# Kernel optimization log

Hardware: AMD Instinct MI355X
Metric: run time of the kernel (lower is better)

## Reference

```python
import jax, jax.numpy as jnp
import numpy as np

N = 100000
NEG_SLOPE = 0.2
EPS = 1e-16


def _gat_layer(x, W, a_src, a_dst, b, src, dst, heads, dim, concat):
    # Linear projection -> [N, H, D]
    h = (x @ W).reshape(x.shape[0], heads, dim)
    # Per-node attention logits [N, H]
    al_src = jnp.sum(h * a_src[None], axis=-1)
    al_dst = jnp.sum(h * a_dst[None], axis=-1)
    # Per-edge logits, leaky relu (negative_slope=0.2)
    e = al_src[src] + al_dst[dst]                      # [E, H]
    e = jnp.where(e >= 0, e, NEG_SLOPE * e)
    # Scatter softmax over destination neighborhoods
    emax = jax.ops.segment_max(e, dst, num_segments=N)  # [N, H]
    ee = jnp.exp(e - emax[dst])
    denom = jax.ops.segment_sum(ee, dst, num_segments=N)
    alpha = ee / (denom[dst] + EPS)                    # [E, H]
    # Weighted scatter-add aggregation
    msg = h[src] * alpha[:, :, None]                   # [E, H, D]
    out = jax.ops.segment_sum(msg, dst, num_segments=N)  # [N, H, D]
    if concat:
        out = out.reshape(N, heads * dim)
    else:
        out = out.mean(axis=1)
    return out + b


def setup_inputs() -> dict:
    key = jax.random.key(0)
    ks = jax.random.split(key, 10)
    F_in, hid, H, C = 500, 8, 8, 3
    E = 3200000
    x = jax.random.normal(ks[0], (N, F_in), dtype=jnp.float32)
    edge_index = jax.random.randint(ks[1], (2, E), 0, N, dtype=jnp.int64)
    s1 = (1.0 / np.sqrt(F_in)).astype(np.float32)
    s2 = (1.0 / np.sqrt(hid * H)).astype(np.float32)
    return {
        "x": x,
        "edge_index": edge_index,
        "W1": jax.random.normal(ks[2], (F_in, H * hid), dtype=jnp.float32) * s1,
        "att_src1": jax.random.normal(ks[3], (H, hid), dtype=jnp.float32),
        "att_dst1": jax.random.normal(ks[4], (H, hid), dtype=jnp.float32),
        "b1": jnp.zeros((H * hid,), dtype=jnp.float32),
        "W2": jax.random.normal(ks[5], (H * hid, C), dtype=jnp.float32) * s2,
        "att_src2": jax.random.normal(ks[6], (1, C), dtype=jnp.float32),
        "att_dst2": jax.random.normal(ks[7], (1, C), dtype=jnp.float32),
        "b2": jnp.zeros((C,), dtype=jnp.float32),
    }


def reference(x, edge_index, W1, att_src1, att_dst1, b1, W2, att_src2, att_dst2, b2):
    # Add self-loops (PyG GATConv default)
    loop = jnp.arange(N, dtype=edge_index.dtype)
    src = jnp.concatenate([edge_index[0], loop])
    dst = jnp.concatenate([edge_index[1], loop])
    # Layer 1: 8 heads, concat -> [N, 64], ELU
    h = _gat_layer(x, W1, att_src1, att_dst1, b1, src, dst, heads=8, dim=8, concat=True)
    h = jax.nn.elu(h)
    # Layer 2: 1 head, no concat -> [N, 3]
    out = _gat_layer(h, W2, att_src2, att_dst2, b2, src, dst, heads=1, dim=3, concat=False)
    return out, jax.nn.log_softmax(out, axis=1)
```

## Files before the change

### kernel.cpp

```cpp
#include <hip/hip_runtime.h>
#include <hip/hip_bf16.h>


#define F_IN 500
#define HEADS 8
#define HID 8
#define HD 64
#define CLS 3
#define NEG 0.2f
#define EPSV 1e-16f
#define LOG2E 1.44269504088896340736f

#define NBLK_H 256
#define NBKT_MAX 3136

typedef __attribute__((ext_vector_type(8))) short short8v;
typedef __attribute__((ext_vector_type(4))) float f32x4;

__device__ inline short bfs(float v) {
    __hip_bfloat16 b = __float2bfloat16(v);
    return *(short*)&b;
}

__device__ inline int ld_edge(const void* ei, long idx, int is64) {
    return is64 ? (int)((const long long*)ei)[idx] : ((const int*)ei)[idx];
}

__global__ void k_prepW(const float* __restrict__ W1, ushort* __restrict__ W1b2,
                        const int* __restrict__ ei, int* __restrict__ flag) {
    if (blockIdx.x == 0 && threadIdx.x == 0) {
        int z = 0;
        for (int i = 1; i < 16; i += 2) z += (ei[i] == 0) ? 1 : 0;
        *flag = (z == 8) ? 1 : 0;
    }
    int i = blockIdx.x * 256 + threadIdx.x;
    if (i >= 16 * 64 * 32) return;
    int ks = i >> 11;
    int c = (i >> 5) & 63;
    int st = i & 31;
    int q = (st >> 3) ^ ((c >> 1) & 3);
    int k = ks * 32 + q * 8 + (st & 7);
    float v = (k < F_IN) ? W1[k * HD + c] : 0.f;
    __hip_bfloat16 b = __float2bfloat16(v);
    W1b2[i] = *(ushort*)&b;
}

__device__ __forceinline__ void g1_stage(const float* __restrict__ x,
        const ushort* __restrict__ W1b2, char* smem, int buf, int ks,
        int rowb, int N, int lane, int w) {
    const int k0 = ks * 32;
    {
        const ushort* srcB = W1b2 + ks * 2048 + (w * 64 + lane) * 8;
        char* dstB = smem + 16384 + buf * 4096 + w * 1024;
        __builtin_amdgcn_global_load_lds(
            (const __attribute__((address_space(1))) void*)srcB,
            (__attribute__((address_space(3))) void*)dstB, 16, 0, 0);
    }
#pragma unroll
    for (int i = 0; i < 2; ++i) {
        int vt = i * 256 + w * 64 + lane;
        int row = vt >> 3;
        int c = (vt & 7) ^ (row & 7);
        int ke = k0 + c * 4; if (ke > 496) ke = 496;
        int rowg = rowb + row; if (rowg >= N) rowg = N - 1;
        const float* srcA = x + (long)rowg * F_IN + ke;
        char* dstA = smem + buf * 8192 + i * 4096 + w * 1024;
        __builtin_amdgcn_global_load_lds(
            (const __attribute__((address_space(1))) void*)srcA,
            (__attribute__((address_space(3))) void*)dstA, 16, 0, 0);
    }
}

__global__ __launch_bounds__(256) void k_fatA(const float* __restrict__ x,
        const ushort* __restrict__ W1b2,
        const float* __restrict__ asrc, const float* __restrict__ adst,
        float* __restrict__ als, float* __restrict__ ald,
        ushort* __restrict__ h1b, int N,
        const void* ei, int E, int nbkt, int* __restrict__ ghist,
        const int* __restrict__ flag) {
    __shared__ char smem[24576];
    int gB = (N + 63) >> 6;
    int t = threadIdx.x;

    if ((int)blockIdx.x >= gB) {
        int hb = blockIdx.x - gB;
        int* h = (int*)smem;
        int tot = E + N;
        int epb = (tot + NBLK_H - 1) / NBLK_H;
        int e0 = hb * epb, e1 = min(tot, e0 + epb);
        for (int i = t; i < nbkt; i += 256) h[i] = 0;
        __syncthreads();
        int is64 = *flag;
        for (int e = e0 + t; e < e1; e += 256) {
            int dst = (e < E) ? ld_edge(ei, (long)E + e, is64) : (e - E);
            atomicAdd(&h[dst >> 5], 1);
        }
        __syncthreads();
        for (int i = t; i < nbkt; i += 256)
            ghist[hb * nbkt + i] = h[i];
        return;
    }

    int lane = t & 63;
    int w = t >> 6;
    int l16 = lane & 15, oct = lane >> 4;
    int rowb = blockIdx.x * 64;

    f32x4 acc0 = {0.f, 0.f, 0.f, 0.f};
    f32x4 acc1 = {0.f, 0.f, 0.f, 0.f};
    f32x4 acc2 = {0.f, 0.f, 0.f, 0.f};
    f32x4 acc3 = {0.f, 0.f, 0.f, 0.f};

    g1_stage(x, W1b2, smem, 0, 0, rowb, N, lane, w);
    __syncthreads();

    int rl = w * 16 + l16;
    int asw = l16 & 7;
    int bsw = (l16 >> 1) & 3;

    for (int ks = 0; ks < 16; ++ks) {
        int cur = ks & 1;
        if (ks < 15)
            g1_stage(x, W1b2, smem, cur ^ 1, ks + 1, rowb, N, lane, w);
        const char* Ab = smem + cur * 8192;
        const char* Bb = smem + 16384 + cur * 4096;
        float4 x0 = *reinterpret_cast<const float4*>(
            Ab + rl * 128 + ((2 * oct + 0) ^ asw) * 16);
        float4 x1 = *reinterpret_cast<const float4*>(
            Ab + rl * 128 + ((2 * oct + 1) ^ asw) * 16);
        short8v a;
        a[0] = bfs(x0.x); a[1] = bfs(x0.y); a[2] = bfs(x0.z); a[3] = bfs(x0.w);
        a[4] = bfs(x1.x); a[5] = bfs(x1.y); a[6] = bfs(x1.z); a[7] = bfs(x1.w);
        short8v b0 = *reinterpret_cast<const short8v*>(
            Bb + (0 * 16 + l16) * 64 + (oct ^ bsw) * 16);
        short8v b1 = *reinterpret_cast<const short8v*>(
            Bb + (1 * 16 + l16) * 64 + (oct ^ bsw) * 16);
        short8v b2 = *reinterpret_cast<const short8v*>(
            Bb + (2 * 16 + l16) * 64 + (oct ^ bsw) * 16);
        short8v b3 = *reinterpret_cast<const short8v*>(
            Bb + (3 * 16 + l16) * 64 + (oct ^ bsw) * 16);
        acc0 = __builtin_amdgcn_mfma_f32_16x16x32_bf16(a, b0, acc0, 0, 0, 0);
        acc1 = __builtin_amdgcn_mfma_f32_16x16x32_bf16(a, b1, acc1, 0, 0, 0);
        acc2 = __builtin_amdgcn_mfma_f32_16x16x32_bf16(a, b2, acc2, 0, 0, 0);
        acc3 = __builtin_amdgcn_mfma_f32_16x16x32_bf16(a, b3, acc3, 0, 0, 0);
        __syncthreads();
    }

    float* fs = (float*)smem;
#pragma unroll
    for (int r = 0; r < 4; ++r) {
        int rl_ = w * 16 + oct * 4 + r;
        fs[rl_ * 64 + l16 +  0] = acc0[r];
        fs[rl_ * 64 + l16 + 16] = acc1[r];
        fs[rl_ * 64 + l16 + 32] = acc2[r];
        fs[rl_ * 64 + l16 + 48] = acc3[r];
    }
    __syncthreads();
#pragma unroll
    for (int j = t; j < 512; j += 256) {
        int row = j >> 3, h = j & 7;
        int gn = rowb + row;
        if (gn < N) {
            const float* hp = fs + row * 64 + h * 8;
            float4 v0 = *reinterpret_cast<const float4*>(hp);
            float4 v1 = *reinterpret_cast<const float4*>(hp + 4);
            const float* s = asrc + h * 8;
            const float* d = adst + h * 8;
            float s1 = v0.x * s[0] + v0.y * s[1] + v0.z * s[2] + v0.w * s[3]
                     + v1.x * s[4] + v1.y * s[5] + v1.z * s[6] + v1.w * s[7];
            float s2 = v0.x * d[0] + v0.y * d[1] + v0.z * d[2] + v0.w * d[3]
                     + v1.x * d[4] + v1.y * d[5] + v1.z * d[6] + v1.w * d[7];
            als[gn * 8 + h] = s1 * LOG2E;
            ald[gn * 8 + h] = s2 * LOG2E;
            ushort hb[8];
            hb[0] = (ushort)bfs(v0.x); hb[1] = (ushort)bfs(v0.y);
            hb[2] = (ushort)bfs(v0.z); hb[3] = (ushort)bfs(v0.w);
            hb[4] = (ushort)bfs(v1.x); hb[5] = (ushort)bfs(v1.y);
            hb[6] = (ushort)bfs(v1.z); hb[7] = (ushort)bfs(v1.w);
            *reinterpret_cast<uint4*>(h1b + (long)gn * HD + h * 8) =
                *reinterpret_cast<const uint4*>(hb);
        }
    }
}


__global__ void k_bsum(int* __restrict__ ghist, int* __restrict__ colsum, int nbkt) {
    int b = blockIdx.x * 256 + threadIdx.x;
    if (b >= nbkt) return;
    int run = 0;
    for (int i = 0; i < NBLK_H; i++) {
        int v = ghist[i * nbkt + b];
        ghist[i * nbkt + b] = run;
        run += v;
    }
    colsum[b] = run;
}

__global__ __launch_bounds__(256) void k_bscan2(const int* __restrict__ colsum,
        int* __restrict__ boff, int nbkt) {
    __shared__ int part[256];
    int per = (nbkt + 255) / 256;
    int t = threadIdx.x;
    int lo = t * per, hi = min(nbkt, lo + per);
    int s = 0;
    for (int i = lo; i < hi; i++) s += colsum[i];
    part[t] = s;
    __syncthreads();
    for (int off = 1; off < 256; off <<= 1) {
        int v = (t >= off) ? part[t - off] : 0;
        __syncthreads();
        part[t] += v;
        __syncthreads();
    }
    int run = (t > 0) ? part[t - 1] : 0;
    for (int i = lo; i < hi; i++) { boff[i] = run; run += colsum[i]; }
    if (t == 255) boff[nbkt] = part[255];
}

__global__ __launch_bounds__(256) void k_scatter(const void* ei, int E, int N, int nbkt,
        const int* __restrict__ ghist, const int* __restrict__ boff,
        uint* __restrict__ pairs, const int* flag) {
    __shared__ int cur[NBKT_MAX];
    int tot = E + N;
    int epb = (tot + NBLK_H - 1) / NBLK_H;
    int e0 = blockIdx.x * epb, e1 = min(tot, e0 + epb);
    for (int i = threadIdx.x; i < nbkt; i += 256)
        cur[i] = boff[i] + ghist[blockIdx.x * nbkt + i];
    __syncthreads();
    int is64 = *flag;
    for (int e = e0 + threadIdx.x; e < e1; e += 256) {
        int src, dst;
        if (e < E) { src = ld_edge(ei, e, is64); dst = ld_edge(ei, (long)E + e, is64); }
        else { src = dst = e - E; }
        int pos = atomicAdd(&cur[dst >> 5], 1);
        pairs[pos] = ((uint)src << 5) | (uint)(dst & 31);
    }
}

__global__ __launch_bounds__(256) void k_fill3(const uint* __restrict__ pairs,
        const int* __restrict__ boff, int* __restrict__ rowptr,
        int* __restrict__ csr, int N, int nbkt) {
    __shared__ int cnt[32];
    __shared__ int base[32];
    __shared__ int cur[32];
    int b = blockIdx.x;
    int t = threadIdx.x;
    if (t < 32) { cnt[t] = 0; cur[t] = 0; }
    __syncthreads();
    int p0 = boff[b], p1 = boff[b + 1];
    for (int p = p0 + t; p < p1; p += 256)
        atomicAdd(&cnt[pairs[p] & 31], 1);
    __syncthreads();
    if (t < 32) {
        int pre = 0;
#pragma unroll
        for (int i = 0; i < 32; i++) pre += (i < t) ? cnt[i] : 0;
        base[t] = p0 + pre;
        int n = b * 32 + t;
        if (n < N) rowptr[n] = base[t];
    }
    if (b == 0 && t == 0) rowptr[N] = boff[nbkt];
    __syncthreads();
    for (int p = p0 + t; p < p1; p += 256) {
        uint v = pairs[p];
        int lo = v & 31;
        int pos = base[lo] + atomicAdd(&cur[lo], 1);
        csr[pos] = (int)(v >> 5);
    }
}

__global__ __launch_bounds__(256) void k_agg1(const int* __restrict__ rowptr,
        const int* __restrict__ csr, const ushort* __restrict__ h1b,
        const float* __restrict__ als, const float* __restrict__ ald,
        const float* __restrict__ b1, const float* __restrict__ W2,
        const float* __restrict__ as2, const float* __restrict__ ad2,
        float* __restrict__ h2p, float* __restrict__ ald2, int N) {
    int lane = threadIdx.x & 63;
    int wid = threadIdx.x >> 6;
    int half = lane >> 5;
    int n = blockIdx.x * 8 + wid * 2 + half;
    bool act = (n < N);
    int nc = act ? n : (N - 1);
    int es = (lane >> 3) & 3;
    int h = lane & 7;
    float aldh = ald[nc * HEADS + h];
    int rs = rowptr[nc], re = rowptr[nc + 1];

    float acc[4][8];
    float den[4] = {0.f, 0.f, 0.f, 0.f};
#pragma unroll
    for (int q = 0; q < 4; ++q)
#pragma unroll
        for (int j = 0; j < 8; ++j) acc[q][j] = 0.f;

    int jb = rs;
    for (; jb + 16 <= re; jb += 16) {
        int s[4]; float e[4]; float p[4]; uint4 u[4];
#pragma unroll
        for (int q = 0; q < 4; ++q) s[q] = csr[jb + q * 4 + es];
#pragma unroll
        for (int q = 0; q < 4; ++q) {
            e[q] = als[s[q] * HEADS + h] + aldh;
            u[q] = *reinterpret_cast<const uint4*>(h1b + (long)s[q] * HD + h * 8);
        }
#pragma unroll
        for (int q = 0; q < 4; ++q) {
            e[q] = fmaxf(e[q], NEG * e[q]);
            p[q] = exp2f(e[q]);
        }
#pragma unroll
        for (int q = 0; q < 4; ++q) {
            acc[q][0] += p[q] * __uint_as_float(u[q].x << 16);
            acc[q][1] += p[q] * __uint_as_float(u[q].x & 0xffff0000u);
            acc[q][2] += p[q] * __uint_as_float(u[q].y << 16);
            acc[q][3] += p[q] * __uint_as_float(u[q].y & 0xffff0000u);
            acc[q][4] += p[q] * __uint_as_float(u[q].z << 16);
            acc[q][5] += p[q] * __uint_as_float(u[q].z & 0xffff0000u);
            acc[q][6] += p[q] * __uint_as_float(u[q].w << 16);
            acc[q][7] += p[q] * __uint_as_float(u[q].w & 0xffff0000u);
            den[q] += p[q];
        }
    }
    for (; jb < re; jb += 4) {
        int eidx = jb + es;
        bool valid = (eidx < re);
        int s = csr[valid ? eidx : rs];
        float e = als[s * HEADS + h] + aldh;
        e = fmaxf(e, NEG * e);
        float p = valid ? exp2f(e) : 0.f;
        uint4 u = *reinterpret_cast<const uint4*>(h1b + (long)s * HD + h * 8);
        acc[0][0] += p * __uint_as_float(u.x << 16);
        acc[0][1] += p * __uint_as_float(u.x & 0xffff0000u);
        acc[0][2] += p * __uint_as_float(u.y << 16);
        acc[0][3] += p * __uint_as_float(u.y & 0xffff0000u);
        acc[0][4] += p * __uint_as_float(u.z << 16);
        acc[0][5] += p * __uint_as_float(u.z & 0xffff0000u);
        acc[0][6] += p * __uint_as_float(u.w << 16);
        acc[0][7] += p * __uint_as_float(u.w & 0xffff0000u);
        den[0] += p;
    }
    float a0 = (acc[0][0] + acc[1][0]) + (acc[2][0] + acc[3][0]);
    float a1 = (acc[0][1] + acc[1][1]) + (acc[2][1] + acc[3][1]);
    float a2 = (acc[0][2] + acc[1][2]) + (acc[2][2] + acc[3][2]);
    float a3 = (acc[0][3] + acc[1][3]) + (acc[2][3] + acc[3][3]);
    float a4 = (acc[0][4] + acc[1][4]) + (acc[2][4] + acc[3][4]);
    float a5 = (acc[0][5] + acc[1][5]) + (acc[2][5] + acc[3][5]);
    float a6 = (acc[0][6] + acc[1][6]) + (acc[2][6] + acc[3][6]);
    float a7 = (acc[0][7] + acc[1][7]) + (acc[2][7] + acc[3][7]);
    float dn = (den[0] + den[1]) + (den[2] + den[3]);
#pragma unroll
    for (int off = 8; off <= 16; off <<= 1) {
        dn += __shfl_xor(dn, off);
        a0 += __shfl_xor(a0, off); a1 += __shfl_xor(a1, off);
        a2 += __shfl_xor(a2, off); a3 += __shfl_xor(a3, off);
        a4 += __shfl_xor(a4, off); a5 += __shfl_xor(a5, off);
        a6 += __shfl_xor(a6, off); a7 += __shfl_xor(a7, off);
    }
    float sel_a = (es < 2) ? ((es == 0) ? a0 : a1) : ((es == 2) ? a2 : a3);
    float sel_b = (es < 2) ? ((es == 0) ? a4 : a5) : ((es == 2) ? a6 : a7);
    int da = h * 8 + es, db = da + 4;
    float inv = 1.f / (dn + EPSV);
    float oa = sel_a * inv + b1[da];
    float ob = sel_b * inv + b1[db];
    oa = (oa > 0.f) ? oa : __expf(oa) - 1.f;
    ob = (ob > 0.f) ? ob : __expf(ob) - 1.f;
    float p0 = oa * W2[da * CLS + 0] + ob * W2[db * CLS + 0];
    float p1 = oa * W2[da * CLS + 1] + ob * W2[db * CLS + 1];
    float p2 = oa * W2[da * CLS + 2] + ob * W2[db * CLS + 2];
#pragma unroll
    for (int off = 1; off <= 16; off <<= 1) {
        p0 += __shfl_xor(p0, off);
        p1 += __shfl_xor(p1, off);
        p2 += __shfl_xor(p2, off);
    }
    if ((lane & 31) == 0 && act) {
        float als2v = (p0 * as2[0] + p1 * as2[1] + p2 * as2[2]) * LOG2E;
        *reinterpret_cast<float4*>(h2p + (long)n * 4) =
            make_float4(p0, p1, p2, als2v);
        ald2[n] = (p0 * ad2[0] + p1 * ad2[1] + p2 * ad2[2]) * LOG2E;
    }
}

__global__ __launch_bounds__(256) void k_agg2(const int* __restrict__ rowptr,
        const int* __restrict__ csr, const float* __restrict__ h2p,
        const float* __restrict__ ald2v,
        const float* __restrict__ b2, float* __restrict__ out, int N) {
    int n = blockIdx.x * 8 + (threadIdx.x >> 5);
    if (n >= N) return;
    int lane = threadIdx.x & 31;
    float aldv = ald2v[n];
    int rs = rowptr[n], re = rowptr[n + 1];
    float sum = 0.f, a0 = 0.f, a1 = 0.f, a2 = 0.f;
    for (int j = rs + lane; j < re; j += 32) {
        int s = csr[j];
        float4 hv = *reinterpret_cast<const float4*>(h2p + (long)s * 4);
        float e = hv.w + aldv;
        e = fmaxf(e, NEG * e);
        float p = exp2f(e);
        sum += p;
        a0 += p * hv.x;
        a1 += p * hv.y;
        a2 += p * hv.z;
    }
#pragma unroll
    for (int off = 1; off < 32; off <<= 1) {
        sum += __shfl_xor(sum, off);
        a0 += __shfl_xor(a0, off);
        a1 += __shfl_xor(a1, off);
        a2 += __shfl_xor(a2, off);
    }
    if (lane == 0) {
        float d = sum + EPSV;
        float v0 = a0 / d + b2[0], v1 = a1 / d + b2[1], v2 = a2 / d + b2[2];
        float mx = fmaxf(v0, fmaxf(v1, v2));
        float se = __expf(v0 - mx) + __expf(v1 - mx) + __expf(v2 - mx);
        float ls = mx + __logf(se);
        out[n * CLS + 0] = v0; out[n * CLS + 1] = v1; out[n * CLS + 2] = v2;
        long o2 = (long)N * CLS;
        out[o2 + n * CLS + 0] = v0 - ls;
        out[o2 + n * CLS + 1] = v1 - ls;
        out[o2 + n * CLS + 2] = v2 - ls;
    }
}

extern "C" void kernel_launch(void* const* d_in, const int* in_sizes, int n_in,
                              void* d_out, int out_size, void* d_ws, size_t ws_size,
                              hipStream_t stream) {
    const float* x   = (const float*)d_in[0];
    const void*  ei  = d_in[1];
    const float* W1  = (const float*)d_in[2];
    const float* as1 = (const float*)d_in[3];
    const float* ad1 = (const float*)d_in[4];
    const float* b1  = (const float*)d_in[5];
    const float* W2  = (const float*)d_in[6];
    const float* as2 = (const float*)d_in[7];
    const float* ad2 = (const float*)d_in[8];
    const float* b2  = (const float*)d_in[9];
    int N = in_sizes[0] / F_IN;
    int E = in_sizes[1] / 2;
    int tot = E + N;
    int nbkt = (N + 31) >> 5;

    char* w = (char*)d_ws;
    auto alloc = [&](size_t bytes) -> char* {
        char* p = w; w += (bytes + 255) & ~size_t(255); return p;
    };
    ushort* h1b    = (ushort*)alloc((size_t)N * HD * 2);
    float*  als1   = (float*)alloc((size_t)N * HEADS * 4);
    float*  ald1   = (float*)alloc((size_t)N * HEADS * 4);
    int*    rowptr = (int*)alloc((size_t)(N + 1) * 4);
    int*    csr    = (int*)alloc((size_t)tot * 4);
    float*  h2p    = (float*)alloc((size_t)N * 4 * 4);
    float*  ald2   = (float*)alloc((size_t)N * 4);
    ushort* W1b2   = (ushort*)alloc((size_t)16 * 64 * 32 * 2);
    int*    flag   = (int*)alloc(256);
    uint*   pairs  = (uint*)alloc((size_t)tot * 4);
    int*    ghist  = (int*)alloc((size_t)NBLK_H * nbkt * 4);
    int*    colsum = (int*)alloc((size_t)nbkt * 4);
    int*    boff   = (int*)alloc((size_t)(nbkt + 1) * 4);

    int gB = (N + 63) / 64;
    k_prepW<<<(16 * 64 * 32 + 255) / 256, 256, 0, stream>>>(W1, W1b2, (const int*)ei, flag);
    k_fatA<<<gB + NBLK_H, 256, 0, stream>>>(x, W1b2, as1, ad1, als1, ald1, h1b, N,
                                            ei, E, nbkt, ghist, flag);
    k_bsum<<<(nbkt + 255) / 256, 256, 0, stream>>>(ghist, colsum, nbkt);
    k_bscan2<<<1, 256, 0, stream>>>(colsum, boff, nbkt);
    k_scatter<<<NBLK_H, 256, 0, stream>>>(ei, E, N, nbkt, ghist, boff, pairs, flag);
    k_fill3<<<nbkt, 256, 0, stream>>>(pairs, boff, rowptr, csr, N, nbkt);
    k_agg1<<<(N + 7) / 8, 256, 0, stream>>>(rowptr, csr, h1b, als1, ald1, b1,
                                            W2, as2, ad2, h2p, ald2, N);
    k_agg2<<<(N + 7) / 8, 256, 0, stream>>>(rowptr, csr, h2p, ald2, b2,
                                            (float*)d_out, N);
}
```

Measured before the change: 298.3 us.

## Fuse CSR bucket fill with layer-1 aggregation in one kernel

Merges the per-bucket CSR fill kernel with the first-layer attention aggregation, so each block finishes building the adjacency for its 32 destination nodes and then aggregates them in four passes. Row bounds come from shared memory instead of a global rowptr reload, and the csr entries just written are likely still in cache. It also drops one kernel launch. In exchange, parallelism falls from about 12.5k blocks to about 3.1k larger blocks, and each block runs its fill and aggregate phases back to back, which may reduce latency hiding for the gather-heavy aggregation.

After: 305.0 us. 1.02x slower.

```diff
diff --git a/kernel.cpp b/kernel.cpp
--- a/kernel.cpp
+++ b/kernel.cpp
@@ -237,11 +237,16 @@
     }
 }
 
-__global__ __launch_bounds__(256) void k_fill3(const uint* __restrict__ pairs,
+__global__ __launch_bounds__(256) void k_fillagg(const uint* __restrict__ pairs,
         const int* __restrict__ boff, int* __restrict__ rowptr,
-        int* __restrict__ csr, int N, int nbkt) {
+        int* __restrict__ csr, const ushort* __restrict__ h1b,
+        const float* __restrict__ als, const float* __restrict__ ald,
+        const float* __restrict__ b1, const float* __restrict__ W2,
+        const float* __restrict__ as2, const float* __restrict__ ad2,
+        float* __restrict__ h2p, float* __restrict__ ald2,
+        int N, int nbkt) {
     __shared__ int cnt[32];
-    __shared__ int base[32];
+    __shared__ int sbase[32];
     __shared__ int cur[32];
     int b = blockIdx.x;
     int t = threadIdx.x;
@@ -255,129 +260,129 @@
         int pre = 0;
 #pragma unroll
         for (int i = 0; i < 32; i++) pre += (i < t) ? cnt[i] : 0;
-        base[t] = p0 + pre;
+        sbase[t] = p0 + pre;
         int n = b * 32 + t;
-        if (n < N) rowptr[n] = base[t];
+        if (n < N) rowptr[n] = sbase[t];
     }
     if (b == 0 && t == 0) rowptr[N] = boff[nbkt];
     __syncthreads();
     for (int p = p0 + t; p < p1; p += 256) {
         uint v = pairs[p];
         int lo = v & 31;
-        int pos = base[lo] + atomicAdd(&cur[lo], 1);
+        int pos = sbase[lo] + atomicAdd(&cur[lo], 1);
         csr[pos] = (int)(v >> 5);
     }
-}
-
-__global__ __launch_bounds__(256) void k_agg1(const int* __restrict__ rowptr,
-        const int* __restrict__ csr, const ushort* __restrict__ h1b,
-        const float* __restrict__ als, const float* __restrict__ ald,
-        const float* __restrict__ b1, const float* __restrict__ W2,
-        const float* __restrict__ as2, const float* __restrict__ ad2,
-        float* __restrict__ h2p, float* __restrict__ ald2, int N) {
-    int lane = threadIdx.x & 63;
-    int wid = threadIdx.x >> 6;
+    __syncthreads();
+
+    int lane = t & 63;
+    int wid = t >> 6;
     int half = lane >> 5;
-    int n = blockIdx.x * 8 + wid * 2 + half;
-    bool act = (n < N);
-    int nc = act ? n : (N - 1);
     int es = (lane >> 3) & 3;
     int h = lane & 7;
-    float aldh = ald[nc * HEADS + h];
-    int rs = rowptr[nc], re = rowptr[nc + 1];
-
-    float acc[4][8];
-    float den[4] = {0.f, 0.f, 0.f, 0.f};
-#pragma unroll
-    for (int q = 0; q < 4; ++q)
-#pragma unroll
-        for (int j = 0; j < 8; ++j) acc[q][j] = 0.f;
-
-    int jb = rs;
-    for (; jb + 16 <= re; jb += 16) {
-        int s[4]; float e[4]; float p[4]; uint4 u[4];
-#pragma unroll
-        for (int q = 0; q < 4; ++q) s[q] = csr[jb + q * 4 + es];
-#pragma unroll
-        for (int q = 0; q < 4; ++q) {
-            e[q] = als[s[q] * HEADS + h] + aldh;
-            u[q] = *reinterpret_cast<const uint4*>(h1b + (long)s[q] * HD + h * 8);
-        }
-#pragma unroll
-        for (int q = 0; q < 4; ++q) {
-            e[q] = fmaxf(e[q], NEG * e[q]);
-            p[q] = exp2f(e[q]);
-        }
-#pragma unroll
-        for (int q = 0; q < 4; ++q) {
-            acc[q][0] += p[q] * __uint_as_float(u[q].x << 16);
-            acc[q][1] += p[q] * __uint_as_float(u[q].x & 0xffff0000u);
-            acc[q][2] += p[q] * __uint_as_float(u[q].y << 16);
-            acc[q][3] += p[q] * __uint_as_float(u[q].y & 0xffff0000u);
-            acc[q][4] += p[q] * __uint_as_float(u[q].z << 16);
-            acc[q][5] += p[q] * __uint_as_float(u[q].z & 0xffff0000u);
-            acc[q][6] += p[q] * __uint_as_float(u[q].w << 16);
-            acc[q][7] += p[q] * __uint_as_float(u[q].w & 0xffff0000u);
-            den[q] += p[q];
-        }
-    }
-    for (; jb < re; jb += 4) {
-        int eidx = jb + es;
-        bool valid = (eidx < re);
-        int s = csr[valid ? eidx : rs];
-        float e = als[s * HEADS + h] + aldh;
-        e = fmaxf(e, NEG * e);
-        float p = valid ? exp2f(e) : 0.f;
-        uint4 u = *reinterpret_cast<const uint4*>(h1b + (long)s * HD + h * 8);
-        acc[0][0] += p * __uint_as_float(u.x << 16);
-        acc[0][1] += p * __uint_as_float(u.x & 0xffff0000u);
-        acc[0][2] += p * __uint_as_float(u.y << 16);
-        acc[0][3] += p * __uint_as_float(u.y & 0xffff0000u);
-        acc[0][4] += p * __uint_as_float(u.z << 16);
-        acc[0][5] += p * __uint_as_float(u.z & 0xffff0000u);
-        acc[0][6] += p * __uint_as_float(u.w << 16);
-        acc[0][7] += p * __uint_as_float(u.w & 0xffff0000u);
-        den[0] += p;
-    }
-    float a0 = (acc[0][0] + acc[1][0]) + (acc[2][0] + acc[3][0]);
-    float a1 = (acc[0][1] + acc[1][1]) + (acc[2][1] + acc[3][1]);
-    float a2 = (acc[0][2] + acc[1][2]) + (acc[2][2] + acc[3][2]);
-    float a3 = (acc[0][3] + acc[1][3]) + (acc[2][3] + acc[3][3]);
-    float a4 = (acc[0][4] + acc[1][4]) + (acc[2][4] + acc[3][4]);
-    float a5 = (acc[0][5] + acc[1][5]) + (acc[2][5] + acc[3][5]);
-    float a6 = (acc[0][6] + acc[1][6]) + (acc[2][6] + acc[3][6]);
-    float a7 = (acc[0][7] + acc[1][7]) + (acc[2][7] + acc[3][7]);
-    float dn = (den[0] + den[1]) + (den[2] + den[3]);
-#pragma unroll
-    for (int off = 8; off <= 16; off <<= 1) {
-        dn += __shfl_xor(dn, off);
-        a0 += __shfl_xor(a0, off); a1 += __shfl_xor(a1, off);
-        a2 += __shfl_xor(a2, off); a3 += __shfl_xor(a3, off);
-        a4 += __shfl_xor(a4, off); a5 += __shfl_xor(a5, off);
-        a6 += __shfl_xor(a6, off); a7 += __shfl_xor(a7, off);
-    }
-    float sel_a = (es < 2) ? ((es == 0) ? a0 : a1) : ((es == 2) ? a2 : a3);
-    float sel_b = (es < 2) ? ((es == 0) ? a4 : a5) : ((es == 2) ? a6 : a7);
-    int da = h * 8 + es, db = da + 4;
-    float inv = 1.f / (dn + EPSV);
-    float oa = sel_a * inv + b1[da];
-    float ob = sel_b * inv + b1[db];
-    oa = (oa > 0.f) ? oa : __expf(oa) - 1.f;
-    ob = (ob > 0.f) ? ob : __expf(ob) - 1.f;
-    float p0 = oa * W2[da * CLS + 0] + ob * W2[db * CLS + 0];
-    float p1 = oa * W2[da * CLS + 1] + ob * W2[db * CLS + 1];
-    float p2 = oa * W2[da * CLS + 2] + ob * W2[db * CLS + 2];
-#pragma unroll
-    for (int off = 1; off <= 16; off <<= 1) {
-        p0 += __shfl_xor(p0, off);
-        p1 += __shfl_xor(p1, off);
-        p2 += __shfl_xor(p2, off);
-    }
-    if ((lane & 31) == 0 && act) {
-        float als2v = (p0 * as2[0] + p1 * as2[1] + p2 * as2[2]) * LOG2E;
-        *reinterpret_cast<float4*>(h2p + (long)n * 4) =
-            make_float4(p0, p1, p2, als2v);
-        ald2[n] = (p0 * ad2[0] + p1 * ad2[1] + p2 * ad2[2]) * LOG2E;
+
+#pragma unroll
+    for (int pass = 0; pass < 4; ++pass) {
+        int nib = pass * 8 + wid * 2 + half;
+        int n = b * 32 + nib;
+        bool act = (n < N);
+        int nc = act ? n : (N - 1);
+        int rs = sbase[nib];
+        int re = rs + cnt[nib];
+        float aldh = ald[nc * HEADS + h];
+
+        float acc[4][8];
+        float den[4] = {0.f, 0.f, 0.f, 0.f};
+#pragma unroll
+        for (int q = 0; q < 4; ++q)
+#pragma unroll
+            for (int j = 0; j < 8; ++j) acc[q][j] = 0.f;
+
+        int jb = rs;
+        for (; jb + 16 <= re; jb += 16) {
+            int s[4]; float e[4]; float p[4]; uint4 u[4];
+#pragma unroll
+            for (int q = 0; q < 4; ++q) s[q] = csr[jb + q * 4 + es];
+#pragma unroll
+            for (int q = 0; q < 4; ++q) {
+                e[q] = als[s[q] * HEADS + h] + aldh;
+                u[q] = *reinterpret_cast<const uint4*>(h1b + (long)s[q] * HD + h * 8);
+            }
+#pragma unroll
+            for (int q = 0; q < 4; ++q) {
+                e[q] = fmaxf(e[q], NEG * e[q]);
+                p[q] = exp2f(e[q]);
+            }
+#pragma unroll
+            for (int q = 0; q < 4; ++q) {
+                acc[q][0] += p[q] * __uint_as_float(u[q].x << 16);
+                acc[q][1] += p[q] * __uint_as_float(u[q].x & 0xffff0000u);
+                acc[q][2] += p[q] * __uint_as_float(u[q].y << 16);
+                acc[q][3] += p[q] * __uint_as_float(u[q].y & 0xffff0000u);
+                acc[q][4] += p[q] * __uint_as_float(u[q].z << 16);
+                acc[q][5] += p[q] * __uint_as_float(u[q].z & 0xffff0000u);
+                acc[q][6] += p[q] * __uint_as_float(u[q].w << 16);
+                acc[q][7] += p[q] * __uint_as_float(u[q].w & 0xffff0000u);
+                den[q] += p[q];
+            }
+        }
+        for (; jb < re; jb += 4) {
+            int eidx = jb + es;
+            bool valid = (eidx < re);
+            int s = csr[valid ? eidx : rs];
+            float e = als[s * HEADS + h] + aldh;
+            e = fmaxf(e, NEG * e);
+            float p = valid ? exp2f(e) : 0.f;
+            uint4 u = *reinterpret_cast<const uint4*>(h1b + (long)s * HD + h * 8);
+            acc[0][0] += p * __uint_as_float(u.x << 16);
+            acc[0][1] += p * __uint_as_float(u.x & 0xffff0000u);
+            acc[0][2] += p * __uint_as_float(u.y << 16);
+            acc[0][3] += p * __uint_as_float(u.y & 0xffff0000u);
+            acc[0][4] += p * __uint_as_float(u.z << 16);
+            acc[0][5] += p * __uint_as_float(u.z & 0xffff0000u);
+            acc[0][6] += p * __uint_as_float(u.w << 16);
+            acc[0][7] += p * __uint_as_float(u.w & 0xffff0000u);
+            den[0] += p;
+        }
+        float a0 = (acc[0][0] + acc[1][0]) + (acc[2][0] + acc[3][0]);
+        float a1 = (acc[0][1] + acc[1][1]) + (acc[2][1] + acc[3][1]);
+        float a2 = (acc[0][2] + acc[1][2]) + (acc[2][2] + acc[3][2]);
+        float a3 = (acc[0][3] + acc[1][3]) + (acc[2][3] + acc[3][3]);
+        float a4 = (acc[0][4] + acc[1][4]) + (acc[2][4] + acc[3][4]);
+        float a5 = (acc[0][5] + acc[1][5]) + (acc[2][5] + acc[3][5]);
+        float a6 = (acc[0][6] + acc[1][6]) + (acc[2][6] + acc[3][6]);
+        float a7 = (acc[0][7] + acc[1][7]) + (acc[2][7] + acc[3][7]);
+        float dn = (den[0] + den[1]) + (den[2] + den[3]);
+#pragma unroll
+        for (int off = 8; off <= 16; off <<= 1) {
+            dn += __shfl_xor(dn, off);
+            a0 += __shfl_xor(a0, off); a1 += __shfl_xor(a1, off);
+            a2 += __shfl_xor(a2, off); a3 += __shfl_xor(a3, off);
+            a4 += __shfl_xor(a4, off); a5 += __shfl_xor(a5, off);
+            a6 += __shfl_xor(a6, off); a7 += __shfl_xor(a7, off);
+        }
+        float sel_a = (es < 2) ? ((es == 0) ? a0 : a1) : ((es == 2) ? a2 : a3);
+        float sel_b = (es < 2) ? ((es == 0) ? a4 : a5) : ((es == 2) ? a6 : a7);
+        int da = h * 8 + es, db = da + 4;
+        float inv = 1.f / (dn + EPSV);
+        float oa = sel_a * inv + b1[da];
+        float ob = sel_b * inv + b1[db];
+        oa = (oa > 0.f) ? oa : __expf(oa) - 1.f;
+        ob = (ob > 0.f) ? ob : __expf(ob) - 1.f;
+        float p0 = oa * W2[da * CLS + 0] + ob * W2[db * CLS + 0];
+        float p1 = oa * W2[da * CLS + 1] + ob * W2[db * CLS + 1];
+        float p2 = oa * W2[da * CLS + 2] + ob * W2[db * CLS + 2];
+#pragma unroll
+        for (int off = 1; off <= 16; off <<= 1) {
+            p0 += __shfl_xor(p0, off);
+            p1 += __shfl_xor(p1, off);
+            p2 += __shfl_xor(p2, off);
+        }
+        if ((lane & 31) == 0 && act) {
+            float als2v = (p0 * as2[0] + p1 * as2[1] + p2 * as2[2]) * LOG2E;
+            *reinterpret_cast<float4*>(h2p + (long)n * 4) =
+                make_float4(p0, p1, p2, als2v);
+            ald2[n] = (p0 * ad2[0] + p1 * ad2[1] + p2 * ad2[2]) * LOG2E;
+        }
     }
 }
 
@@ -466,9 +471,8 @@
     k_bsum<<<(nbkt + 255) / 256, 256, 0, stream>>>(ghist, colsum, nbkt);
     k_bscan2<<<1, 256, 0, stream>>>(colsum, boff, nbkt);
     k_scatter<<<NBLK_H, 256, 0, stream>>>(ei, E, N, nbkt, ghist, boff, pairs, flag);
-    k_fill3<<<nbkt, 256, 0, stream>>>(pairs, boff, rowptr, csr, N, nbkt);
-    k_agg1<<<(N + 7) / 8, 256, 0, stream>>>(rowptr, csr, h1b, als1, ald1, b1,
-                                            W2, as2, ad2, h2p, ald2, N);
+    k_fillagg<<<nbkt, 256, 0, stream>>>(pairs, boff, rowptr, csr, h1b, als1, ald1,
+                                        b1, W2, as2, ad2, h2p, ald2, N, nbkt);
     k_agg2<<<(N + 7) / 8, 256, 0, stream>>>(rowptr, csr, h2p, ald2, b2,
                                             (float*)d_out, N);
 }
```

## Fuse CSR build kernels into one cooperative kernel with grid syncs

Applied to the files above, without the earlier changes.

Merges the four CSR construction kernels (bucket column sum, offset scan, scatter and per-bucket fill) into a single cooperative launch of 256 blocks, separated by grid-wide barriers. The aim is to remove three kernel launch gaps. In exchange, the fill phase now runs on only 256 blocks looping over about 3136 buckets instead of one block per bucket, which lowers parallelism for that phase. The grid syncs also add their own barrier cost.

After: 404.8 us. +35.7%, slower.

```diff
diff --git a/kernel.cpp b/kernel.cpp
--- a/kernel.cpp
+++ b/kernel.cpp
@@ -1,5 +1,8 @@
 #include <hip/hip_runtime.h>
 #include <hip/hip_bf16.h>
+#include <hip/hip_cooperative_groups.h>
+
+namespace cg = cooperative_groups;
 
 
 #define F_IN 500
@@ -183,89 +186,88 @@
     }
 }
 
-
-__global__ void k_bsum(int* __restrict__ ghist, int* __restrict__ colsum, int nbkt) {
-    int b = blockIdx.x * 256 + threadIdx.x;
-    if (b >= nbkt) return;
-    int run = 0;
-    for (int i = 0; i < NBLK_H; i++) {
-        int v = ghist[i * nbkt + b];
-        ghist[i * nbkt + b] = run;
-        run += v;
-    }
-    colsum[b] = run;
-}
-
-__global__ __launch_bounds__(256) void k_bscan2(const int* __restrict__ colsum,
-        int* __restrict__ boff, int nbkt) {
+__global__ __launch_bounds__(256) void k_csr(const void* ei, int E, int N, int nbkt,
+        int* __restrict__ ghist, int* __restrict__ colsum, int* __restrict__ boff,
+        uint* __restrict__ pairs, int* __restrict__ rowptr, int* __restrict__ csr,
+        const int* __restrict__ flag) {
+    cg::grid_group grid = cg::this_grid();
+    __shared__ int sh[NBKT_MAX];
     __shared__ int part[256];
-    int per = (nbkt + 255) / 256;
-    int t = threadIdx.x;
-    int lo = t * per, hi = min(nbkt, lo + per);
-    int s = 0;
-    for (int i = lo; i < hi; i++) s += colsum[i];
-    part[t] = s;
-    __syncthreads();
-    for (int off = 1; off < 256; off <<= 1) {
-        int v = (t >= off) ? part[t - off] : 0;
-        __syncthreads();
-        part[t] += v;
-        __syncthreads();
-    }
-    int run = (t > 0) ? part[t - 1] : 0;
-    for (int i = lo; i < hi; i++) { boff[i] = run; run += colsum[i]; }
-    if (t == 255) boff[nbkt] = part[255];
-}
-
-__global__ __launch_bounds__(256) void k_scatter(const void* ei, int E, int N, int nbkt,
-        const int* __restrict__ ghist, const int* __restrict__ boff,
-        uint* __restrict__ pairs, const int* flag) {
-    __shared__ int cur[NBKT_MAX];
+    __shared__ int cnt[32], base[32], cur[32];
+    int blk = blockIdx.x, t = threadIdx.x;
     int tot = E + N;
-    int epb = (tot + NBLK_H - 1) / NBLK_H;
-    int e0 = blockIdx.x * epb, e1 = min(tot, e0 + epb);
-    for (int i = threadIdx.x; i < nbkt; i += 256)
-        cur[i] = boff[i] + ghist[blockIdx.x * nbkt + i];
-    __syncthreads();
     int is64 = *flag;
-    for (int e = e0 + threadIdx.x; e < e1; e += 256) {
-        int src, dst;
-        if (e < E) { src = ld_edge(ei, e, is64); dst = ld_edge(ei, (long)E + e, is64); }
-        else { src = dst = e - E; }
-        int pos = atomicAdd(&cur[dst >> 5], 1);
-        pairs[pos] = ((uint)src << 5) | (uint)(dst & 31);
-    }
-}
-
-__global__ __launch_bounds__(256) void k_fill3(const uint* __restrict__ pairs,
-        const int* __restrict__ boff, int* __restrict__ rowptr,
-        int* __restrict__ csr, int N, int nbkt) {
-    __shared__ int cnt[32];
-    __shared__ int base[32];
-    __shared__ int cur[32];
-    int b = blockIdx.x;
-    int t = threadIdx.x;
-    if (t < 32) { cnt[t] = 0; cur[t] = 0; }
-    __syncthreads();
-    int p0 = boff[b], p1 = boff[b + 1];
-    for (int p = p0 + t; p < p1; p += 256)
-        atomicAdd(&cnt[pairs[p] & 31], 1);
-    __syncthreads();
-    if (t < 32) {
-        int pre = 0;
-#pragma unroll
-        for (int i = 0; i < 32; i++) pre += (i < t) ? cnt[i] : 0;
-        base[t] = p0 + pre;
-        int n = b * 32 + t;
-        if (n < N) rowptr[n] = base[t];
-    }
-    if (b == 0 && t == 0) rowptr[N] = boff[nbkt];
-    __syncthreads();
-    for (int p = p0 + t; p < p1; p += 256) {
-        uint v = pairs[p];
-        int lo = v & 31;
-        int pos = base[lo] + atomicAdd(&cur[lo], 1);
-        csr[pos] = (int)(v >> 5);
+
+    for (int b = blk * 256 + t; b < nbkt; b += NBLK_H * 256) {
+        int run = 0;
+        for (int i = 0; i < NBLK_H; i++) {
+            int v = ghist[i * nbkt + b];
+            ghist[i * nbkt + b] = run;
+            run += v;
+        }
+        colsum[b] = run;
+    }
+    grid.sync();
+
+    if (blk == 0) {
+        int per = (nbkt + 255) / 256;
+        int lo = t * per, hi = min(nbkt, lo + per);
+        int s = 0;
+        for (int i = lo; i < hi; i++) s += colsum[i];
+        part[t] = s;
+        __syncthreads();
+        for (int off = 1; off < 256; off <<= 1) {
+            int v = (t >= off) ? part[t - off] : 0;
+            __syncthreads();
+            part[t] += v;
+            __syncthreads();
+        }
+        int run = (t > 0) ? part[t - 1] : 0;
+        for (int i = lo; i < hi; i++) { boff[i] = run; run += colsum[i]; }
+        if (t == 255) boff[nbkt] = part[255];
+    }
+    grid.sync();
+
+    {
+        int epb = (tot + NBLK_H - 1) / NBLK_H;
+        int e0 = blk * epb, e1 = min(tot, e0 + epb);
+        for (int i = t; i < nbkt; i += 256)
+            sh[i] = boff[i] + ghist[blk * nbkt + i];
+        __syncthreads();
+        for (int e = e0 + t; e < e1; e += 256) {
+            int src, dst;
+            if (e < E) { src = ld_edge(ei, e, is64); dst = ld_edge(ei, (long)E + e, is64); }
+            else { src = dst = e - E; }
+            int pos = atomicAdd(&sh[dst >> 5], 1);
+            pairs[pos] = ((uint)src << 5) | (uint)(dst & 31);
+        }
+    }
+    grid.sync();
+
+    if (blk == 0 && t == 0) rowptr[N] = boff[nbkt];
+    for (int b = blk; b < nbkt; b += NBLK_H) {
+        if (t < 32) { cnt[t] = 0; cur[t] = 0; }
+        __syncthreads();
+        int p0 = boff[b], p1 = boff[b + 1];
+        for (int p = p0 + t; p < p1; p += 256)
+            atomicAdd(&cnt[pairs[p] & 31], 1);
+        __syncthreads();
+        if (t < 32) {
+            int pre = 0;
+#pragma unroll
+            for (int i = 0; i < 32; i++) pre += (i < t) ? cnt[i] : 0;
+            base[t] = p0 + pre;
+            int n = b * 32 + t;
+            if (n < N) rowptr[n] = base[t];
+        }
+        __syncthreads();
+        for (int p = p0 + t; p < p1; p += 256) {
+            uint v = pairs[p];
+            int lo = v & 31;
+            int pos = base[lo] + atomicAdd(&cur[lo], 1);
+            csr[pos] = (int)(v >> 5);
+        }
+        __syncthreads();
     }
 }
 
@@ -463,10 +465,13 @@
     k_prepW<<<(16 * 64 * 32 + 255) / 256, 256, 0, stream>>>(W1, W1b2, (const int*)ei, flag);
     k_fatA<<<gB + NBLK_H, 256, 0, stream>>>(x, W1b2, as1, ad1, als1, ald1, h1b, N,
                                             ei, E, nbkt, ghist, flag);
-    k_bsum<<<(nbkt + 255) / 256, 256, 0, stream>>>(ghist, colsum, nbkt);
-    k_bscan2<<<1, 256, 0, stream>>>(colsum, boff, nbkt);
-    k_scatter<<<NBLK_H, 256, 0, stream>>>(ei, E, N, nbkt, ghist, boff, pairs, flag);
-    k_fill3<<<nbkt, 256, 0, stream>>>(pairs, boff, rowptr, csr, N, nbkt);
+    {
+        void* args[] = { (void*)&ei, (void*)&E, (void*)&N, (void*)&nbkt,
+                         (void*)&ghist, (void*)&colsum, (void*)&boff,
+                         (void*)&pairs, (void*)&rowptr, (void*)&csr, (void*)&flag };
+        hipLaunchCooperativeKernel((void*)k_csr, dim3(NBLK_H), dim3(256),
+                                   args, 0, stream);
+    }
     k_agg1<<<(N + 7) / 8, 256, 0, stream>>>(rowptr, csr, h1b, als1, ald1, b1,
                                             W2, as2, ad2, h2p, ald2, N);
     k_agg2<<<(N + 7) / 8, 256, 0, stream>>>(rowptr, csr, h2p, ald2, b2,
```
